# Kernel optimization log

Hardware: AMD Instinct MI355X
Metric: run time of the kernel (lower is better)

## Reference

```python
import jax, jax.numpy as jnp
import numpy as np

B, D = 8192, 2048
H1, H2, G = 1024, 512, 512
T, SPEC, SH = 2, 2, 2
E = T * SPEC + SH          # total experts = 6
EC = SPEC + SH             # experts per task = 4


def setup_inputs() -> dict:
    key = jax.random.key(0)
    ks = jax.random.split(key, 6)
    s = 0.02  # glorot-ish scale
    return {
        "x":   jax.random.normal(ks[0], (B, D), jnp.float32),
        "We1": jax.random.normal(ks[1], (E, D, H1), jnp.float32) * s,
        "be1": jnp.zeros((E, H1), jnp.float32),
        "We2": jax.random.normal(ks[2], (E, H1, H2), jnp.float32) * s,
        "be2": jnp.zeros((E, H2), jnp.float32),
        "Wg1": jax.random.normal(ks[3], (T, D, G), jnp.float32) * s,
        "bg1": jnp.zeros((T, G), jnp.float32),
        "Wgs": jax.random.normal(ks[4], (T, G, EC), jnp.float32) * s,
    }


# per-task expert indices: task i uses its SPEC specific experts + the SH shared (last) experts
_IDX = np.array([[i * SPEC + j for j in range(SPEC)] + list(range(T * SPEC, E))
                 for i in range(T)])  # [T, EC]


def reference(x, We1, be1, We2, be2, Wg1, bg1, Wgs):
    # All experts batched into grouped GEMMs (the fusion the original loop misses)
    h1 = jax.nn.relu(jnp.einsum('bd,edh->beh', x, We1) + be1)        # [B,E,H1]
    h2 = jax.nn.relu(jnp.einsum('beh,eho->beo', h1, We2) + be2)      # [B,E,H2]
    # Gate MLP per task, batched over tasks
    g = jax.nn.relu(jnp.einsum('bd,tdg->btg', x, Wg1) + bg1)         # [B,T,G]
    gate = jax.nn.softmax(jnp.einsum('btg,tge->bte', g, Wgs), axis=-1)  # [B,T,EC]
    sel = h2[:, _IDX, :]                                             # [B,T,EC,H2]
    out = jnp.einsum('bteo,bte->tbo', sel, gate)                     # [T,B,H2]
    return out
```

## Files before the change

kernel.cpp:

```cpp
#include <hip/hip_runtime.h>
#include <hip/hip_bf16.h>
#include <cstdint>
#include <cstddef>

#define B_   8192
#define D_   2048
#define H1_  1024
#define H2_  512
#define G_   512
#define T_   2
#define E_   6
#define EC_  4

typedef __bf16 bf16_t;
typedef __attribute__((ext_vector_type(8))) __bf16 bf16x8;
typedef __attribute__((ext_vector_type(4))) float f32x4;

__device__ __forceinline__ void gload_lds16(const bf16_t* g, bf16_t* l) {
    __builtin_amdgcn_global_load_lds(
        (const __attribute__((address_space(1))) bf16_t*)g,
        (__attribute__((address_space(3))) bf16_t*)l,
        16, 0, 0);
}

__global__ __launch_bounds__(256) void cast_x_kernel(
    const float* __restrict__ src, bf16_t* __restrict__ dst, int n8)
{
    int i = blockIdx.x * blockDim.x + threadIdx.x;
    if (i >= n8) return;
    const float4* s = (const float4*)src + (size_t)i * 2;
    float4 a = s[0], b = s[1];
    bf16x8 o;
    o[0] = (bf16_t)a.x; o[1] = (bf16_t)a.y; o[2] = (bf16_t)a.z; o[3] = (bf16_t)a.w;
    o[4] = (bf16_t)b.x; o[5] = (bf16_t)b.y; o[6] = (bf16_t)b.z; o[7] = (bf16_t)b.w;
    *(bf16x8*)(dst + (size_t)i * 8) = o;
}

__global__ __launch_bounds__(256) void transpose_cast_kernel(
    const float* __restrict__ src, bf16_t* __restrict__ dst, int R, int C)
{
    __shared__ float tile[32][33];
    int bz = blockIdx.z;
    src += (size_t)bz * R * C;
    dst += (size_t)bz * R * C;
    int c0 = blockIdx.x * 32, r0 = blockIdx.y * 32;
    int tx = threadIdx.x, ty = threadIdx.y;
#pragma unroll
    for (int i = 0; i < 32; i += 8)
        tile[ty + i][tx] = src[(size_t)(r0 + ty + i) * C + (c0 + tx)];
    __syncthreads();
#pragma unroll
    for (int i = 0; i < 32; i += 8)
        dst[(size_t)(c0 + ty + i) * R + (r0 + tx)] = (bf16_t)tile[tx][ty + i];
}

__global__ __launch_bounds__(512, 2) void gemm256k64_bt_bias_relu(
    const bf16_t* __restrict__ A, const bf16_t* __restrict__ Bt,
    const float* __restrict__ bias, bf16_t* __restrict__ C,
    int M, int N, int K, long long strideA)
{
    const int e = blockIdx.z;
    A    += (size_t)e * (size_t)strideA;
    Bt   += (size_t)e * (size_t)N * (size_t)K;
    bias += (size_t)e * (size_t)N;
    C    += (size_t)e * (size_t)M * (size_t)N;

    const int gx  = gridDim.x;
    const int nwg = gx * gridDim.y;
    const int lin = blockIdx.y * gx + blockIdx.x;
    const int swz = (lin & 7) * (nwg >> 3) + (lin >> 3);
    const int bx  = swz % gx;
    const int by  = swz / gx;
    const int row0 = by * 256;
    const int col0 = bx * 256;

    __shared__ bf16_t lsA[2][16384];
    __shared__ bf16_t lsB[2][16384];

    const int tid  = threadIdx.x;
    const int lane = tid & 63;
    const int wave = tid >> 6;
    const int wr   = wave >> 2;
    const int wc   = wave & 3;

    size_t offG[2];
    int    ldsOff[2];
#pragma unroll
    for (int l = 0; l < 2; ++l) {
        int idx = l * 512 + tid;
        int r   = idx >> 3;
        int c   = (idx & 7) ^ (r & 7);
        offG[l]   = (size_t)r * (size_t)K + (size_t)(c * 8);
        ldsOff[l] = l * 4096 + wave * 512;
    }
    const bf16_t* gA = A  + (size_t)row0 * (size_t)K;
    const bf16_t* gB = Bt + (size_t)col0 * (size_t)K;
    const size_t halfStride = (size_t)128 * (size_t)K;

    const int rbA = (wr * 128 + (lane & 15)) * 64;
    const int rbB = (wc * 64  + (lane & 15)) * 64;
    int xc[2];
#pragma unroll
    for (int ks = 0; ks < 2; ++ks)
        xc[ks] = (ks * 32 + ((lane >> 4) * 8)) ^ ((lane & 7) << 3);

    f32x4 acc[8][4];
#pragma unroll
    for (int m = 0; m < 8; ++m)
#pragma unroll
        for (int n = 0; n < 4; ++n)
            acc[m][n] = (f32x4){0.f, 0.f, 0.f, 0.f};

    const int nt    = K >> 6;
    const int niter = nt >> 1;

#define STAGE_A(dst, kt, h) do {                                              \
    _Pragma("unroll")                                                         \
    for (int l_ = 0; l_ < 2; ++l_)                                            \
        gload_lds16(gA + (size_t)((kt) * 64) + (size_t)(h) * halfStride       \
                       + offG[l_],                                            \
                    &lsA[dst][(h) * 8192 + ldsOff[l_]]);                      \
} while (0)

#define STAGE_B(dst, kt, h) do {                                              \
    _Pragma("unroll")                                                         \
    for (int l_ = 0; l_ < 2; ++l_)                                            \
        gload_lds16(gB + (size_t)((kt) * 64) + (size_t)(h) * halfStride       \
                       + offG[l_],                                            \
                    &lsB[dst][(h) * 8192 + ldsOff[l_]]);                      \
} while (0)

#define PHASE(d, qm, STMT, ENDW) do {                                         \
    bf16x8 af00, af01, af10, af11;                                            \
    af00 = *(const bf16x8*)&lsA[d][rbA + (2*(qm)+0) * 1024 + xc[0]];          \
    af01 = *(const bf16x8*)&lsA[d][rbA + (2*(qm)+0) * 1024 + xc[1]];          \
    af10 = *(const bf16x8*)&lsA[d][rbA + (2*(qm)+1) * 1024 + xc[0]];          \
    af11 = *(const bf16x8*)&lsA[d][rbA + (2*(qm)+1) * 1024 + xc[1]];          \
    if ((qm) == 0) {                                                          \
        _Pragma("unroll")                                                     \
        for (int n_ = 0; n_ < 4; ++n_) {                                      \
            bfr[n_][0] = *(const bf16x8*)&lsB[d][rbB + n_ * 1024 + xc[0]];    \
            bfr[n_][1] = *(const bf16x8*)&lsB[d][rbB + n_ * 1024 + xc[1]];    \
        }                                                                     \
    }                                                                         \
    STMT;                                                                     \
    __builtin_amdgcn_sched_barrier(0);                                        \
    __builtin_amdgcn_s_barrier();                                             \
    asm volatile("s_waitcnt lgkmcnt(0)" ::: "memory");                        \
    __builtin_amdgcn_sched_barrier(0);                                        \
    __builtin_amdgcn_s_setprio(1);                                            \
    _Pragma("unroll")                                                         \
    for (int n_ = 0; n_ < 4; ++n_) {                                          \
        acc[2*(qm)+0][n_] = __builtin_amdgcn_mfma_f32_16x16x32_bf16(          \
                                af00, bfr[n_][0], acc[2*(qm)+0][n_], 0,0,0);  \
        acc[2*(qm)+0][n_] = __builtin_amdgcn_mfma_f32_16x16x32_bf16(          \
                                af01, bfr[n_][1], acc[2*(qm)+0][n_], 0,0,0);  \
        acc[2*(qm)+1][n_] = __builtin_amdgcn_mfma_f32_16x16x32_bf16(          \
                                af10, bfr[n_][0], acc[2*(qm)+1][n_], 0,0,0);  \
        acc[2*(qm)+1][n_] = __builtin_amdgcn_mfma_f32_16x16x32_bf16(          \
                                af11, bfr[n_][1], acc[2*(qm)+1][n_], 0,0,0);  \
    }                                                                         \
    __builtin_amdgcn_s_setprio(0);                                            \
    ENDW;                                                                     \
    __builtin_amdgcn_sched_barrier(0);                                        \
    __builtin_amdgcn_s_barrier();                                             \
} while (0)

    STAGE_B(0, 0, 0); STAGE_B(0, 0, 1);
    STAGE_A(0, 0, 0); STAGE_A(0, 0, 1);
    STAGE_B(1, 1, 0); STAGE_B(1, 1, 1);
    asm volatile("s_waitcnt vmcnt(4)" ::: "memory");
    __builtin_amdgcn_sched_barrier(0);
    __builtin_amdgcn_s_barrier();

    for (int i = 0; i < niter; ++i) {
        const int kt0 = 2 * i, kt1 = 2 * i + 1;
        const bool stg = (i + 1 < niter);
        bf16x8 bfr[4][2];

        PHASE(0, 0, { STAGE_A(1, kt1, 0); }, {});
        PHASE(0, 1, { STAGE_A(1, kt1, 1); }, {});
        PHASE(0, 2, { if (stg) STAGE_B(0, kt0 + 2, 0); }, {});
        PHASE(0, 3, { if (stg) STAGE_B(0, kt0 + 2, 1); },
              { if (stg) { asm volatile("s_waitcnt vmcnt(4)" ::: "memory"); }
                else     { asm volatile("s_waitcnt vmcnt(0)" ::: "memory"); } });
        PHASE(1, 0, { if (stg) STAGE_A(0, kt0 + 2, 0); }, {});
        PHASE(1, 1, { if (stg) STAGE_A(0, kt0 + 2, 1); }, {});
        PHASE(1, 2, { if (stg) STAGE_B(1, kt0 + 3, 0); }, {});
        PHASE(1, 3, { if (stg) STAGE_B(1, kt0 + 3, 1); },
              { if (stg) { asm volatile("s_waitcnt vmcnt(4)" ::: "memory"); } });
    }
#undef PHASE
#undef STAGE_A
#undef STAGE_B

    const int crb = row0 + wr * 128 + ((lane >> 4) << 2);
    const int ccb = col0 + wc * 64  + (lane & 15);
#pragma unroll
    for (int n = 0; n < 4; ++n) {
        const int cc = ccb + n * 16;
        const float bv = bias[cc];
#pragma unroll
        for (int m = 0; m < 8; ++m) {
            const int rb = crb + m * 16;
#pragma unroll
            for (int j = 0; j < 4; ++j) {
                float v = acc[m][n][j] + bv;
                v = v > 0.f ? v : 0.f;
                C[(size_t)(rb + j) * N + cc] = (bf16_t)v;
            }
        }
    }
}

__global__ __launch_bounds__(256) void gemm_bt_bias_relu(
    const bf16_t* __restrict__ A, const bf16_t* __restrict__ Bt,
    const float* __restrict__ bias, bf16_t* __restrict__ C,
    int M, int N, int K, long long strideA)
{
    const int e = blockIdx.z;
    A    += (size_t)e * (size_t)strideA;
    Bt   += (size_t)e * (size_t)N * (size_t)K;
    bias += (size_t)e * (size_t)N;
    C    += (size_t)e * (size_t)M * (size_t)N;

    __shared__ bf16_t lsA[128 * 32];
    __shared__ bf16_t lsB[128 * 32];

    const int tid  = threadIdx.x;
    const int lane = tid & 63;
    const int wave = tid >> 6;
    const int wr   = wave >> 1;
    const int wc   = wave & 1;
    const int row0 = blockIdx.y * 128;
    const int col0 = blockIdx.x * 128;

    int sRow[2], sCol[2];
#pragma unroll
    for (int r = 0; r < 2; ++r) {
        int s = (r * 4 + wave) * 512 + lane * 8;
        sRow[r] = s >> 5;
        sCol[r] = s & 31;
    }

    f32x4 acc[4][4];
#pragma unroll
    for (int m = 0; m < 4; ++m)
#pragma unroll
        for (int n = 0; n < 4; ++n)
            acc[m][n] = (f32x4){0.f, 0.f, 0.f, 0.f};

    const int aRowBase = wr * 64 + (lane & 15);
    const int bRowBase = wc * 64 + (lane & 15);
    const int kcol     = (lane >> 4) * 8;

    for (int k0 = 0; k0 < K; k0 += 32) {
#pragma unroll
        for (int r = 0; r < 2; ++r) {
            gload_lds16(A  + (size_t)(row0 + sRow[r]) * K + (k0 + sCol[r]),
                        lsA + (r * 4 + wave) * 512);
            gload_lds16(Bt + (size_t)(col0 + sRow[r]) * K + (k0 + sCol[r]),
                        lsB + (r * 4 + wave) * 512);
        }
        __syncthreads();

        bf16x8 af[4], bfr[4];
#pragma unroll
        for (int m = 0; m < 4; ++m)
            af[m] = *(const bf16x8*)&lsA[(aRowBase + m * 16) * 32 + kcol];
#pragma unroll
        for (int n = 0; n < 4; ++n)
            bfr[n] = *(const bf16x8*)&lsB[(bRowBase + n * 16) * 32 + kcol];

#pragma unroll
        for (int m = 0; m < 4; ++m)
#pragma unroll
            for (int n = 0; n < 4; ++n)
                acc[m][n] = __builtin_amdgcn_mfma_f32_16x16x32_bf16(
                                af[m], bfr[n], acc[m][n], 0, 0, 0);
        __syncthreads();
    }

    const int crow = row0 + wr * 64 + ((lane >> 4) << 2);
    const int ccol = col0 + wc * 64 + (lane & 15);
#pragma unroll
    for (int n = 0; n < 4; ++n) {
        int cc = ccol + n * 16;
        float bv = bias[cc];
#pragma unroll
        for (int m = 0; m < 4; ++m) {
            int rb = crow + m * 16;
#pragma unroll
            for (int j = 0; j < 4; ++j) {
                float v = acc[m][n][j] + bv;
                v = v > 0.f ? v : 0.f;
                C[(size_t)(rb + j) * N + cc] = (bf16_t)v;
            }
        }
    }
}

__global__ __launch_bounds__(256) void gate_kernel(
    const bf16_t* __restrict__ g, const float* __restrict__ Wgs,
    float* __restrict__ gate)
{
    int wid  = blockIdx.x * 4 + (threadIdx.x >> 6);
    int lane = threadIdx.x & 63;
    int t = wid >> 13;
    const bf16_t* grow = g + (size_t)wid * G_;
    bf16x8 gv = *(const bf16x8*)&grow[lane * 8];
    const float* W = Wgs + (size_t)t * G_ * EC_;
    float a0 = 0.f, a1 = 0.f, a2 = 0.f, a3 = 0.f;
#pragma unroll
    for (int i = 0; i < 8; ++i) {
        float gvf = (float)gv[i];
        const float4 w = *(const float4*)&W[(size_t)(lane * 8 + i) * 4];
        a0 += gvf * w.x; a1 += gvf * w.y; a2 += gvf * w.z; a3 += gvf * w.w;
    }
#pragma unroll
    for (int off = 32; off; off >>= 1) {
        a0 += __shfl_xor(a0, off);
        a1 += __shfl_xor(a1, off);
        a2 += __shfl_xor(a2, off);
        a3 += __shfl_xor(a3, off);
    }
    if (lane == 0) {
        float m  = fmaxf(fmaxf(a0, a1), fmaxf(a2, a3));
        float e0 = expf(a0 - m), e1 = expf(a1 - m), e2 = expf(a2 - m), e3 = expf(a3 - m);
        float inv = 1.f / (e0 + e1 + e2 + e3);
        *(float4*)&gate[(size_t)wid * 4] = make_float4(e0 * inv, e1 * inv, e2 * inv, e3 * inv);
    }
}

__global__ __launch_bounds__(256) void combine_kernel(
    const bf16_t* __restrict__ h2, const float* __restrict__ gate,
    float* __restrict__ out)
{
    size_t idx = (size_t)blockIdx.x * 256 + threadIdx.x;
    size_t tb  = idx >> 6;
    int    o0  = (int)(idx & 63) * 8;
    int    t   = (int)(tb >> 13);
    size_t b   = tb & (size_t)(B_ - 1);
    const float4 gv = *(const float4*)&gate[tb * 4];
    const bf16x8 v0 = *(const bf16x8*)&h2[((size_t)(2 * t)     * B_ + b) * H2_ + o0];
    const bf16x8 v1 = *(const bf16x8*)&h2[((size_t)(2 * t + 1) * B_ + b) * H2_ + o0];
    const bf16x8 v2 = *(const bf16x8*)&h2[((size_t)4           * B_ + b) * H2_ + o0];
    const bf16x8 v3 = *(const bf16x8*)&h2[((size_t)5           * B_ + b) * H2_ + o0];
    float r[8];
#pragma unroll
    for (int i = 0; i < 8; ++i)
        r[i] = gv.x * (float)v0[i] + gv.y * (float)v1[i]
             + gv.z * (float)v2[i] + gv.w * (float)v3[i];
    float4* op = (float4*)&out[tb * H2_ + o0];
    op[0] = make_float4(r[0], r[1], r[2], r[3]);
    op[1] = make_float4(r[4], r[5], r[6], r[7]);
}

extern "C" void kernel_launch(void* const* d_in, const int* in_sizes, int n_in,
                              void* d_out, int out_size, void* d_ws, size_t ws_size,
                              hipStream_t stream)
{
    const float* x   = (const float*)d_in[0];
    const float* We1 = (const float*)d_in[1];
    const float* be1 = (const float*)d_in[2];
    const float* We2 = (const float*)d_in[3];
    const float* be2 = (const float*)d_in[4];
    const float* Wg1 = (const float*)d_in[5];
    const float* bg1 = (const float*)d_in[6];
    const float* Wgs = (const float*)d_in[7];
    float* out = (float*)d_out;

    char* ws = (char*)d_ws;
    bf16_t* x_bf = (bf16_t*)ws;  ws += (size_t)B_ * D_ * 2;
    bf16_t* w1t  = (bf16_t*)ws;  ws += (size_t)E_ * H1_ * D_ * 2;
    bf16_t* w2t  = (bf16_t*)ws;  ws += (size_t)E_ * H2_ * H1_ * 2;
    bf16_t* wgt  = (bf16_t*)ws;  ws += (size_t)T_ * G_ * D_ * 2;
    bf16_t* h1   = (bf16_t*)ws;  ws += (size_t)E_ * B_ * H1_ * 2;
    bf16_t* h2   = (bf16_t*)ws;  ws += (size_t)E_ * B_ * H2_ * 2;
    bf16_t* gbuf = (bf16_t*)ws;  ws += (size_t)T_ * B_ * G_ * 2;
    float*  gate = (float*)ws;   ws += (size_t)T_ * B_ * EC_ * 4;

    cast_x_kernel<<<(B_ * D_ / 8) / 256, 256, 0, stream>>>(x, x_bf, B_ * D_ / 8);
    dim3 tb(32, 8);
    transpose_cast_kernel<<<dim3(H1_ / 32, D_ / 32, E_),  tb, 0, stream>>>(We1, w1t, D_,  H1_);
    transpose_cast_kernel<<<dim3(H2_ / 32, H1_ / 32, E_), tb, 0, stream>>>(We2, w2t, H1_, H2_);
    transpose_cast_kernel<<<dim3(G_ / 32, D_ / 32, T_),   tb, 0, stream>>>(Wg1, wgt, D_,  G_);

    gemm256k64_bt_bias_relu<<<dim3(H1_ / 256, B_ / 256, E_), 512, 0, stream>>>(
        x_bf, w1t, be1, h1, B_, H1_, D_, 0LL);
    gemm256k64_bt_bias_relu<<<dim3(H2_ / 256, B_ / 256, E_), 512, 0, stream>>>(
        h1, w2t, be2, h2, B_, H2_, H1_, (long long)B_ * H1_);

    gemm_bt_bias_relu<<<dim3(G_ / 128, B_ / 128, T_), 256, 0, stream>>>(
        x_bf, wgt, bg1, gbuf, B_, G_, D_, 0LL);

    gate_kernel<<<(T_ * B_) / 4, 256, 0, stream>>>(gbuf, Wgs, gate);
    combine_kernel<<<((size_t)T_ * B_ * H2_ / 8) / 256, 256, 0, stream>>>(h2, gate, out);
}
```

Before: 408.3 us.

## Fold gate GEMM into layer-1 grouped GEMM and retile layer-2 GEMM

The two gate weight matrices are stored as a seventh 1024-wide 'expert' slab next to the expert weights, with biases concatenated, so the first-layer grouped GEMM computes the gate hidden layer as well and the separate gate GEMM launch disappears. The gate kernel now reads its inputs from that extra slab of h1. Layer 2 switches to a new 128x256-tile kernel with a 3-stage LDS ring, XOR-swizzled loads and tile swizzling. The 256-tile kernel's phase loop also drops its trailing barrier and moves the vmcnt wait earlier. These changes add two small device memcpys and carry some risk of synchronization hazards from the removed barrier.

New measurement: 383.8 us. -6.0%, faster.

```diff
diff --git a/kernel.cpp b/kernel.cpp
--- a/kernel.cpp
+++ b/kernel.cpp
@@ -54,7 +54,7 @@
         dst[(size_t)(c0 + ty + i) * R + (r0 + tx)] = (bf16_t)tile[tx][ty + i];
 }
 
-__global__ __launch_bounds__(512, 2) void gemm256k64_bt_bias_relu(
+__global__ __launch_bounds__(512, 2) void gemm256_8p1b(
     const bf16_t* __restrict__ A, const bf16_t* __restrict__ Bt,
     const float* __restrict__ bias, bf16_t* __restrict__ C,
     int M, int N, int K, long long strideA)
@@ -130,7 +130,7 @@
                     &lsB[dst][(h) * 8192 + ldsOff[l_]]);                      \
 } while (0)
 
-#define PHASE(d, qm, STMT, ENDW) do {                                         \
+#define PHASE(d, qm, STMT, WAITV) do {                                        \
     bf16x8 af00, af01, af10, af11;                                            \
     af00 = *(const bf16x8*)&lsA[d][rbA + (2*(qm)+0) * 1024 + xc[0]];          \
     af01 = *(const bf16x8*)&lsA[d][rbA + (2*(qm)+0) * 1024 + xc[1]];          \
@@ -144,6 +144,7 @@
         }                                                                     \
     }                                                                         \
     STMT;                                                                     \
+    WAITV;                                                                    \
     __builtin_amdgcn_sched_barrier(0);                                        \
     __builtin_amdgcn_s_barrier();                                             \
     asm volatile("s_waitcnt lgkmcnt(0)" ::: "memory");                        \
@@ -161,17 +162,16 @@
                                 af11, bfr[n_][1], acc[2*(qm)+1][n_], 0,0,0);  \
     }                                                                         \
     __builtin_amdgcn_s_setprio(0);                                            \
-    ENDW;                                                                     \
     __builtin_amdgcn_sched_barrier(0);                                        \
-    __builtin_amdgcn_s_barrier();                                             \
 } while (0)
 
+    STAGE_A(0, 0, 0); STAGE_A(0, 0, 1);
     STAGE_B(0, 0, 0); STAGE_B(0, 0, 1);
-    STAGE_A(0, 0, 0); STAGE_A(0, 0, 1);
     STAGE_B(1, 1, 0); STAGE_B(1, 1, 1);
     asm volatile("s_waitcnt vmcnt(4)" ::: "memory");
     __builtin_amdgcn_sched_barrier(0);
     __builtin_amdgcn_s_barrier();
+    __builtin_amdgcn_sched_barrier(0);
 
     for (int i = 0; i < niter; ++i) {
         const int kt0 = 2 * i, kt1 = 2 * i + 1;
@@ -213,7 +213,7 @@
     }
 }
 
-__global__ __launch_bounds__(256) void gemm_bt_bias_relu(
+__global__ __launch_bounds__(512, 4) void gemm_bn256_bias_relu(
     const bf16_t* __restrict__ A, const bf16_t* __restrict__ Bt,
     const float* __restrict__ bias, bf16_t* __restrict__ C,
     int M, int N, int K, long long strideA)
@@ -224,24 +224,41 @@
     bias += (size_t)e * (size_t)N;
     C    += (size_t)e * (size_t)M * (size_t)N;
 
-    __shared__ bf16_t lsA[128 * 32];
-    __shared__ bf16_t lsB[128 * 32];
+    const int gx  = gridDim.x;
+    const int nwg = gx * gridDim.y;
+    const int lin = blockIdx.y * gx + blockIdx.x;
+    const int swz = (lin & 7) * (nwg >> 3) + (lin >> 3);
+    const int row0 = (swz / gx) * 128;
+    const int col0 = (swz % gx) * 256;
+
+    __shared__ bf16_t lsA[3][128 * 32];
+    __shared__ bf16_t lsB[3][256 * 32];
 
     const int tid  = threadIdx.x;
     const int lane = tid & 63;
     const int wave = tid >> 6;
-    const int wr   = wave >> 1;
-    const int wc   = wave & 1;
-    const int row0 = blockIdx.y * 128;
-    const int col0 = blockIdx.x * 128;
-
-    int sRow[2], sCol[2];
-#pragma unroll
-    for (int r = 0; r < 2; ++r) {
-        int s = (r * 4 + wave) * 512 + lane * 8;
-        sRow[r] = s >> 5;
-        sCol[r] = s & 31;
-    }
+    const int wr   = wave >> 2;
+    const int wc   = wave & 3;
+
+    size_t offA, offB0, offB1;
+    {
+        int rA = tid >> 2, pA = tid & 3;
+        offA = (size_t)rA * (size_t)K + (size_t)(((pA ^ (rA >> 1)) & 3) * 8);
+        int r0_ = tid >> 2, p0_ = tid & 3;
+        offB0 = (size_t)r0_ * (size_t)K + (size_t)(((p0_ ^ (r0_ >> 1)) & 3) * 8);
+        int r1_ = (512 + tid) >> 2, p1_ = tid & 3;
+        offB1 = (size_t)r1_ * (size_t)K + (size_t)(((p1_ ^ (r1_ >> 1)) & 3) * 8);
+    }
+    const int ldsA_off = wave * 512;
+    const int ldsB0off = wave * 512;
+    const int ldsB1off = 4096 + wave * 512;
+
+    const bf16_t* gA = A  + (size_t)row0 * (size_t)K;
+    const bf16_t* gB = Bt + (size_t)col0 * (size_t)K;
+
+    const int xch  = ((lane >> 4) ^ ((lane >> 1) & 3)) << 3;
+    const int aoff = (wr * 64 + (lane & 15)) * 32 + xch;
+    const int boff = (wc * 64 + (lane & 15)) * 32 + xch;
 
     f32x4 acc[4][4];
 #pragma unroll
@@ -250,46 +267,62 @@
         for (int n = 0; n < 4; ++n)
             acc[m][n] = (f32x4){0.f, 0.f, 0.f, 0.f};
 
-    const int aRowBase = wr * 64 + (lane & 15);
-    const int bRowBase = wc * 64 + (lane & 15);
-    const int kcol     = (lane >> 4) * 8;
-
-    for (int k0 = 0; k0 < K; k0 += 32) {
-#pragma unroll
-        for (int r = 0; r < 2; ++r) {
-            gload_lds16(A  + (size_t)(row0 + sRow[r]) * K + (k0 + sCol[r]),
-                        lsA + (r * 4 + wave) * 512);
-            gload_lds16(Bt + (size_t)(col0 + sRow[r]) * K + (k0 + sCol[r]),
-                        lsB + (r * 4 + wave) * 512);
-        }
-        __syncthreads();
-
-        bf16x8 af[4], bfr[4];
+    const int nt = K >> 5;
+
+#define STAGE(t_, c_) do {                                                    \
+    const size_t kk_ = (size_t)(t_) * 32;                                     \
+    gload_lds16(gA + kk_ + offA,  &lsA[c_][ldsA_off]);                        \
+    gload_lds16(gB + kk_ + offB0, &lsB[c_][ldsB0off]);                        \
+    gload_lds16(gB + kk_ + offB1, &lsB[c_][ldsB1off]);                        \
+} while (0)
+
+    STAGE(0, 0); STAGE(1, 1); STAGE(2, 2);
+    asm volatile("s_waitcnt vmcnt(6)" ::: "memory");
+    __builtin_amdgcn_s_barrier();
+    __builtin_amdgcn_sched_barrier(0);
+
+    int c = 0;
+    for (int t = 0; t < nt; ++t) {
+        bf16x8 a[4], b[4];
 #pragma unroll
         for (int m = 0; m < 4; ++m)
-            af[m] = *(const bf16x8*)&lsA[(aRowBase + m * 16) * 32 + kcol];
+            a[m] = *(const bf16x8*)&lsA[c][aoff + m * 512];
 #pragma unroll
         for (int n = 0; n < 4; ++n)
-            bfr[n] = *(const bf16x8*)&lsB[(bRowBase + n * 16) * 32 + kcol];
-
+            b[n] = *(const bf16x8*)&lsB[c][boff + n * 512];
+        asm volatile("s_waitcnt lgkmcnt(0)" ::: "memory");
+        __builtin_amdgcn_sched_barrier(0);
+        __builtin_amdgcn_s_barrier();
+        __builtin_amdgcn_sched_barrier(0);
+        if (t + 3 < nt) STAGE(t + 3, c);
+        __builtin_amdgcn_sched_barrier(0);
+        __builtin_amdgcn_s_setprio(1);
 #pragma unroll
         for (int m = 0; m < 4; ++m)
 #pragma unroll
             for (int n = 0; n < 4; ++n)
                 acc[m][n] = __builtin_amdgcn_mfma_f32_16x16x32_bf16(
-                                af[m], bfr[n], acc[m][n], 0, 0, 0);
-        __syncthreads();
-    }
-
-    const int crow = row0 + wr * 64 + ((lane >> 4) << 2);
-    const int ccol = col0 + wc * 64 + (lane & 15);
+                                a[m], b[n], acc[m][n], 0, 0, 0);
+        __builtin_amdgcn_s_setprio(0);
+        __builtin_amdgcn_sched_barrier(0);
+        if (t + 3 < nt) { asm volatile("s_waitcnt vmcnt(6)" ::: "memory"); }
+        else            { asm volatile("s_waitcnt vmcnt(0)" ::: "memory"); }
+        __builtin_amdgcn_sched_barrier(0);
+        __builtin_amdgcn_s_barrier();
+        __builtin_amdgcn_sched_barrier(0);
+        c = (c == 2) ? 0 : c + 1;
+    }
+#undef STAGE
+
+    const int crb = row0 + wr * 64 + ((lane >> 4) << 2);
+    const int ccb = col0 + wc * 64 + (lane & 15);
 #pragma unroll
     for (int n = 0; n < 4; ++n) {
-        int cc = ccol + n * 16;
-        float bv = bias[cc];
+        const int cc = ccb + n * 16;
+        const float bv = bias[cc];
 #pragma unroll
         for (int m = 0; m < 4; ++m) {
-            int rb = crow + m * 16;
+            const int rb = crb + m * 16;
 #pragma unroll
             for (int j = 0; j < 4; ++j) {
                 float v = acc[m][n][j] + bv;
@@ -301,13 +334,14 @@
 }
 
 __global__ __launch_bounds__(256) void gate_kernel(
-    const bf16_t* __restrict__ g, const float* __restrict__ Wgs,
+    const bf16_t* __restrict__ h1, const float* __restrict__ Wgs,
     float* __restrict__ gate)
 {
     int wid  = blockIdx.x * 4 + (threadIdx.x >> 6);
     int lane = threadIdx.x & 63;
     int t = wid >> 13;
-    const bf16_t* grow = g + (size_t)wid * G_;
+    int b = wid & (B_ - 1);
+    const bf16_t* grow = h1 + ((size_t)(6 * B_) + b) * 1024 + t * G_;
     bf16x8 gv = *(const bf16x8*)&grow[lane * 8];
     const float* W = Wgs + (size_t)t * G_ * EC_;
     float a0 = 0.f, a1 = 0.f, a2 = 0.f, a3 = 0.f;
@@ -371,14 +405,20 @@
     float* out = (float*)d_out;
 
     char* ws = (char*)d_ws;
-    bf16_t* x_bf = (bf16_t*)ws;  ws += (size_t)B_ * D_ * 2;
-    bf16_t* w1t  = (bf16_t*)ws;  ws += (size_t)E_ * H1_ * D_ * 2;
-    bf16_t* w2t  = (bf16_t*)ws;  ws += (size_t)E_ * H2_ * H1_ * 2;
-    bf16_t* wgt  = (bf16_t*)ws;  ws += (size_t)T_ * G_ * D_ * 2;
-    bf16_t* h1   = (bf16_t*)ws;  ws += (size_t)E_ * B_ * H1_ * 2;
-    bf16_t* h2   = (bf16_t*)ws;  ws += (size_t)E_ * B_ * H2_ * 2;
-    bf16_t* gbuf = (bf16_t*)ws;  ws += (size_t)T_ * B_ * G_ * 2;
-    float*  gate = (float*)ws;   ws += (size_t)T_ * B_ * EC_ * 4;
+    bf16_t* x_bf  = (bf16_t*)ws;  ws += (size_t)B_ * D_ * 2;
+    bf16_t* w1t   = (bf16_t*)ws;  ws += (size_t)7 * H1_ * D_ * 2;
+    bf16_t* w2t   = (bf16_t*)ws;  ws += (size_t)E_ * H2_ * H1_ * 2;
+    bf16_t* h1    = (bf16_t*)ws;  ws += (size_t)7 * B_ * H1_ * 2;
+    bf16_t* h2    = (bf16_t*)ws;  ws += (size_t)E_ * B_ * H2_ * 2;
+    float*  bias7 = (float*)ws;   ws += (size_t)7 * H1_ * 4;
+    float*  gate  = (float*)ws;   ws += (size_t)T_ * B_ * EC_ * 4;
+
+    bf16_t* wgt = w1t + (size_t)6 * H1_ * D_;
+
+    hipMemcpyAsync(bias7, be1, (size_t)E_ * H1_ * sizeof(float),
+                   hipMemcpyDeviceToDevice, stream);
+    hipMemcpyAsync(bias7 + (size_t)E_ * H1_, bg1, (size_t)T_ * G_ * sizeof(float),
+                   hipMemcpyDeviceToDevice, stream);
 
     cast_x_kernel<<<(B_ * D_ / 8) / 256, 256, 0, stream>>>(x, x_bf, B_ * D_ / 8);
     dim3 tb(32, 8);
@@ -386,14 +426,11 @@
     transpose_cast_kernel<<<dim3(H2_ / 32, H1_ / 32, E_), tb, 0, stream>>>(We2, w2t, H1_, H2_);
     transpose_cast_kernel<<<dim3(G_ / 32, D_ / 32, T_),   tb, 0, stream>>>(Wg1, wgt, D_,  G_);
 
-    gemm256k64_bt_bias_relu<<<dim3(H1_ / 256, B_ / 256, E_), 512, 0, stream>>>(
-        x_bf, w1t, be1, h1, B_, H1_, D_, 0LL);
-    gemm256k64_bt_bias_relu<<<dim3(H2_ / 256, B_ / 256, E_), 512, 0, stream>>>(
+    gemm256_8p1b<<<dim3(H1_ / 256, B_ / 256, 7), 512, 0, stream>>>(
+        x_bf, w1t, bias7, h1, B_, H1_, D_, 0LL);
+    gemm_bn256_bias_relu<<<dim3(H2_ / 256, B_ / 128, E_), 512, 0, stream>>>(
         h1, w2t, be2, h2, B_, H2_, H1_, (long long)B_ * H1_);
 
-    gemm_bt_bias_relu<<<dim3(G_ / 128, B_ / 128, T_), 256, 0, stream>>>(
-        x_bf, wgt, bg1, gbuf, B_, G_, D_, 0LL);
-
-    gate_kernel<<<(T_ * B_) / 4, 256, 0, stream>>>(gbuf, Wgs, gate);
+    gate_kernel<<<(T_ * B_) / 4, 256, 0, stream>>>(h1, Wgs, gate);
     combine_kernel<<<((size_t)T_ * B_ * H2_ / 8) / 256, 256, 0, stream>>>(h2, gate, out);
 }
```
